# Kernel tuning notes

Measured on AMD Instinct MI355X. Metric: run time of the kernel, lower is better.

The kernel has to match this reference:

```python
import jax, jax.numpy as jnp
import numpy as np

NUM_USERS = 100000
NUM_ITEMS = 50000
NUM_EDGES = 2000000
EMBED_DIM = 64


def setup_inputs() -> dict:
    key = jax.random.key(0)
    k1, k2, k3, k4 = jax.random.split(key, 4)
    return {
        "user_emb": jax.random.normal(k1, (NUM_USERS, EMBED_DIM), dtype=jnp.float32),
        "item_emb": jax.random.normal(k2, (NUM_ITEMS, EMBED_DIM), dtype=jnp.float32),
        "edge_values": jnp.ones((NUM_EDGES,), dtype=jnp.float32),
        "edge_users": jax.random.randint(k3, (NUM_EDGES,), 0, NUM_USERS, dtype=jnp.int32),
        "edge_items": jax.random.randint(k4, (NUM_EDGES,), 0, NUM_ITEMS, dtype=jnp.int32),
        "n_layers": 3,
    }


def reference(user_emb, item_emb, edge_values, edge_users, edge_items, n_layers):
    num_users = user_emb.shape[0]
    num_items = item_emb.shape[0]
    n_total = num_users + num_items

    # Row-normalize by user degree: vals * 1/sqrt(row_sum + 1e-6)  (as in create_adj_matrix)
    row_sum = jax.ops.segment_sum(edge_values, edge_users, num_segments=num_users) + 1e-6
    norm_vals = edge_values * (1.0 / jnp.sqrt(row_sum))[edge_users]

    # Symmetric block adjacency: A[u, U+i] = norm_vals, A[U+i, u] = norm_vals
    items_off = edge_items + num_users
    rows = jnp.concatenate([edge_users, items_off])   # [2E] destination nodes
    cols = jnp.concatenate([items_off, edge_users])   # [2E] source nodes
    vals = jnp.concatenate([norm_vals, norm_vals])    # [2E]

    emb0 = jnp.concatenate([user_emb, item_emb], axis=0)  # [N, D]

    def spmm_layer(e, _):
        # out[r] = sum_{edges e: rows==r} vals * e[cols]
        gathered = vals[:, None] * e[cols]  # [2E, D]
        return jax.ops.segment_sum(gathered, rows, num_segments=n_total), None

    emb, _ = jax.lax.scan(spmm_layer, emb0, None, length=n_layers)
    return emb
```

## Files before the change

### kernel.cpp

```cpp
#include <hip/hip_runtime.h>

#define NUM_USERS 100000
#define NUM_ITEMS 50000
#define NUM_EDGES 2000000
#define EMB_D 64
#define N_TOTAL (NUM_USERS + NUM_ITEMS)
#define TOT_ENTRIES (2 * NUM_EDGES)

#define RPB 512
#define NB ((N_TOTAL + RPB - 1) / RPB)
#define EPB 8192
#define PBLK ((NUM_EDGES + EPB - 1) / EPB)
#define HTOT (NB * PBLK)
#define SCAN_BLKS ((HTOT + 255) / 256)

__device__ __forceinline__ unsigned f32_to_bf16_bits(float f) {
    unsigned u = __float_as_uint(f);
    u += 0x7FFFu + ((u >> 16) & 1u);
    return u >> 16;
}

__global__ __launch_bounds__(256) void part_hist_kernel(
        const int* __restrict__ eu, const int* __restrict__ ei,
        int* __restrict__ histT) {
    __shared__ int h[NB];
    const int t = threadIdx.x;
    for (int i = t; i < NB; i += 256) h[i] = 0;
    __syncthreads();
    const int e0 = blockIdx.x * EPB;
    const int e1 = min(e0 + EPB, NUM_EDGES);
    for (int e = e0 + t; e < e1; e += 256) {
        const int u = eu[e];
        const int iu = NUM_USERS + ei[e];
        atomicAdd(&h[u >> 9], 1);
        atomicAdd(&h[iu >> 9], 1);
    }
    __syncthreads();
    for (int i = t; i < NB; i += 256)
        histT[i * PBLK + blockIdx.x] = h[i];
}

__global__ __launch_bounds__(256) void scanA_kernel(int* __restrict__ histT,
                                                    int* __restrict__ bsum) {
    __shared__ int s[256];
    const int t = threadIdx.x;
    const int i = blockIdx.x * 256 + t;
    int v = (i < HTOT) ? histT[i] : 0;
    s[t] = v;
    __syncthreads();
    for (int off = 1; off < 256; off <<= 1) {
        int x = (t >= off) ? s[t - off] : 0;
        __syncthreads();
        s[t] += x;
        __syncthreads();
    }
    if (i < HTOT) histT[i] = s[t] - v;
    if (t == 255) bsum[blockIdx.x] = s[255];
}

__global__ __launch_bounds__(512) void scanB_kernel(int* __restrict__ bsum) {
    __shared__ int s[512];
    const int t = threadIdx.x;
    int v = (t < SCAN_BLKS) ? bsum[t] : 0;
    s[t] = v;
    __syncthreads();
    for (int off = 1; off < 512; off <<= 1) {
        int x = (t >= off) ? s[t - off] : 0;
        __syncthreads();
        s[t] += x;
        __syncthreads();
    }
    if (t < SCAN_BLKS) bsum[t] = s[t] - v;
}

__global__ __launch_bounds__(256) void scanC_kernel(int* __restrict__ histT,
                                                    const int* __restrict__ bsum) {
    const int i = blockIdx.x * 256 + threadIdx.x;
    if (i < HTOT) histT[i] += bsum[blockIdx.x];
}

__global__ __launch_bounds__(256) void part_scatter_kernel(
        const int* __restrict__ eu, const int* __restrict__ ei,
        const int* __restrict__ histT, unsigned* __restrict__ staging) {
    __shared__ int cur[NB];
    const int t = threadIdx.x;
    for (int i = t; i < NB; i += 256) cur[i] = histT[i * PBLK + blockIdx.x];
    __syncthreads();
    const int e0 = blockIdx.x * EPB;
    const int e1 = min(e0 + EPB, NUM_EDGES);
    for (int e = e0 + t; e < e1; e += 256) {
        const int u = eu[e];
        const int iu = NUM_USERS + ei[e];
        const int p1 = atomicAdd(&cur[u >> 9], 1);
        staging[p1] = ((unsigned)(u & 511) << 18) | (unsigned)iu;
        const int p2 = atomicAdd(&cur[iu >> 9], 1);
        staging[p2] = ((unsigned)(iu & 511) << 18) | (unsigned)u;
    }
}

__global__ __launch_bounds__(512) void bucket_finalize_kernel(
        const unsigned* __restrict__ staging,
        const int* __restrict__ histT,
        unsigned* __restrict__ cw,
        int* __restrict__ row_ptr,
        int* __restrict__ cnt_g,
        float* __restrict__ inv_g) {
    __shared__ int sc[512];
    __shared__ int cur[512];
    __shared__ int span[2];
    const int t = threadIdx.x;
    const int b = blockIdx.x;
    if (t == 0) {
        span[0] = histT[b * PBLK];
        span[1] = (b + 1 < NB) ? histT[(b + 1) * PBLK] : TOT_ENTRIES;
    }
    sc[t] = 0;
    __syncthreads();
    const int base = span[0], end = span[1];
    for (int j = base + t; j < end; j += 512)
        atomicAdd(&sc[staging[j] >> 18], 1);
    __syncthreads();
    const int myc = sc[t];
    for (int off = 1; off < 512; off <<= 1) {
        int x = (t >= off) ? sc[t - off] : 0;
        __syncthreads();
        sc[t] += x;
        __syncthreads();
    }
    const int start = base + sc[t] - myc;
    cur[t] = start;
    const int row = b * RPB + t;
    if (row < N_TOTAL) {
        row_ptr[row] = start;
        cnt_g[row] = myc;
        if (row < NUM_USERS) inv_g[row] = rsqrtf((float)myc + 1e-6f);
    }
    __syncthreads();
    for (int j = base + t; j < end; j += 512) {
        const unsigned v = staging[j];
        const int p = atomicAdd(&cur[v >> 18], 1);
        cw[p] = v & 0x3FFFFu;
    }
}

__global__ __launch_bounds__(256) void convert_kernel(
        const float* __restrict__ user_emb,
        const float* __restrict__ item_emb,
        const float* __restrict__ inv,
        unsigned* __restrict__ x0bf) {
    const int tid = blockIdx.x * blockDim.x + threadIdx.x;
    if (tid >= N_TOTAL * (EMB_D / 2)) return;
    const int row = tid >> 5;
    const int d0 = (tid & 31) << 1;
    float f0, f1, sc;
    if (row < NUM_USERS) {
        const float* p = user_emb + (size_t)row * EMB_D + d0;
        f0 = p[0]; f1 = p[1];
        sc = inv[row];
    } else {
        const float* p = item_emb + (size_t)(row - NUM_USERS) * EMB_D + d0;
        f0 = p[0]; f1 = p[1];
        sc = 1.0f;
    }
    f0 *= sc; f1 *= sc;
    x0bf[tid] = f32_to_bf16_bits(f0) | (f32_to_bf16_bits(f1) << 16);
}

template <int FINAL>
__global__ __launch_bounds__(256) void spmm_kernel(
        const uint4* __restrict__ in_bf,
        const int* __restrict__ row_ptr,
        const int* __restrict__ cnt,
        const unsigned* __restrict__ cw,
        const float* __restrict__ inv,
        uint4* __restrict__ out_bf,
        float* __restrict__ out_f32) {
    const int lane = threadIdx.x & 63;
    const int row = blockIdx.x * 4 + (threadIdx.x >> 6);
    if (row >= N_TOTAL) return;

    const int sub = lane >> 3;
    const int l8 = lane & 7;

    const int start = row_ptr[row];
    const int n = cnt[row];

    float acc[8];
    #pragma unroll
    for (int i = 0; i < 8; i++) acc[i] = 0.0f;

    #pragma unroll 2
    for (int k = 0; k < n; k += 8) {
        const int eidx = k + sub;
        const bool valid = (eidx < n);
        const int col = (int)cw[start + (valid ? eidx : 0)];
        const uint4 q = in_bf[(size_t)col * 8 + l8];
        const float w = valid ? 1.0f : 0.0f;
        acc[0] = fmaf(w, __uint_as_float(q.x << 16),         acc[0]);
        acc[1] = fmaf(w, __uint_as_float(q.x & 0xFFFF0000u), acc[1]);
        acc[2] = fmaf(w, __uint_as_float(q.y << 16),         acc[2]);
        acc[3] = fmaf(w, __uint_as_float(q.y & 0xFFFF0000u), acc[3]);
        acc[4] = fmaf(w, __uint_as_float(q.z << 16),         acc[4]);
        acc[5] = fmaf(w, __uint_as_float(q.z & 0xFFFF0000u), acc[5]);
        acc[6] = fmaf(w, __uint_as_float(q.w << 16),         acc[6]);
        acc[7] = fmaf(w, __uint_as_float(q.w & 0xFFFF0000u), acc[7]);
    }

    #pragma unroll
    for (int m = 32; m >= 8; m >>= 1) {
        #pragma unroll
        for (int i = 0; i < 8; i++) acc[i] += __shfl_xor(acc[i], m);
    }

    if (sub == 0) {
        float sc = 1.0f;
        if (row < NUM_USERS) {
            const float iv = inv[row];
            sc = FINAL ? iv : iv * iv;
        }
        #pragma unroll
        for (int i = 0; i < 8; i++) acc[i] *= sc;
        if (FINAL) {
            float4 a = make_float4(acc[0], acc[1], acc[2], acc[3]);
            float4 b = make_float4(acc[4], acc[5], acc[6], acc[7]);
            float* dst = out_f32 + (size_t)row * EMB_D + 8 * l8;
            *reinterpret_cast<float4*>(dst) = a;
            *reinterpret_cast<float4*>(dst + 4) = b;
        } else {
            uint4 h;
            h.x = f32_to_bf16_bits(acc[0]) | (f32_to_bf16_bits(acc[1]) << 16);
            h.y = f32_to_bf16_bits(acc[2]) | (f32_to_bf16_bits(acc[3]) << 16);
            h.z = f32_to_bf16_bits(acc[4]) | (f32_to_bf16_bits(acc[5]) << 16);
            h.w = f32_to_bf16_bits(acc[6]) | (f32_to_bf16_bits(acc[7]) << 16);
            out_bf[(size_t)row * 8 + l8] = h;
        }
    }
}

extern "C" void kernel_launch(void* const* d_in, const int* in_sizes, int n_in,
                              void* d_out, int out_size, void* d_ws, size_t ws_size,
                              hipStream_t stream) {
    const float* user_emb = (const float*)d_in[0];
    const float* item_emb = (const float*)d_in[1];
    const int*   eu       = (const int*)d_in[3];
    const int*   ei       = (const int*)d_in[4];

    float* out = (float*)d_out;

    char* ws = (char*)d_ws;
    size_t off = 0;
    auto alloc = [&](size_t bytes) {
        char* p = ws + off;
        off = (off + bytes + 511) & ~(size_t)511;
        return p;
    };
    int*      histT   = (int*)     alloc((size_t)HTOT * sizeof(int));
    int*      bsum    = (int*)     alloc((size_t)SCAN_BLKS * sizeof(int));
    int*      row_ptr = (int*)     alloc((size_t)N_TOTAL * sizeof(int));
    int*      cnt     = (int*)     alloc((size_t)N_TOTAL * sizeof(int));
    float*    inv     = (float*)   alloc((size_t)NUM_USERS * sizeof(float));
    unsigned* staging = (unsigned*)alloc((size_t)TOT_ENTRIES * sizeof(unsigned));
    unsigned* cw      = (unsigned*)alloc((size_t)TOT_ENTRIES * sizeof(unsigned));
    unsigned* x0bf    = (unsigned*)alloc((size_t)N_TOTAL * EMB_D * 2);
    unsigned* z1      = (unsigned*)alloc((size_t)N_TOTAL * EMB_D * 2);
    unsigned* z2      = (unsigned*)alloc((size_t)N_TOTAL * EMB_D * 2);

    part_hist_kernel<<<PBLK, 256, 0, stream>>>(eu, ei, histT);
    scanA_kernel<<<SCAN_BLKS, 256, 0, stream>>>(histT, bsum);
    scanB_kernel<<<1, 512, 0, stream>>>(bsum);
    scanC_kernel<<<SCAN_BLKS, 256, 0, stream>>>(histT, bsum);
    part_scatter_kernel<<<PBLK, 256, 0, stream>>>(eu, ei, histT, staging);
    bucket_finalize_kernel<<<NB, 512, 0, stream>>>(staging, histT, cw,
                                                   row_ptr, cnt, inv);

    const int cv_threads = N_TOTAL * (EMB_D / 2);
    convert_kernel<<<(cv_threads + 255) / 256, 256, 0, stream>>>(
        user_emb, item_emb, inv, x0bf);

    const int grid = (N_TOTAL + 3) / 4;

    spmm_kernel<0><<<grid, 256, 0, stream>>>((const uint4*)x0bf, row_ptr, cnt,
                                             cw, inv, (uint4*)z1, nullptr);
    spmm_kernel<0><<<grid, 256, 0, stream>>>((const uint4*)z1, row_ptr, cnt,
                                             cw, inv, (uint4*)z2, nullptr);
    spmm_kernel<1><<<grid, 256, 0, stream>>>((const uint4*)z2, row_ptr, cnt,
                                             cw, inv, nullptr, out);
}
```

Baseline: 310.2 us.

## Process four rows per wavefront in SpMM and vectorize embedding conversion

Each wavefront in the SpMM kernel now handles four destination rows at once. Their gathers are interleaved inside one loop over the maximum row length, which raises memory-level parallelism and gives four times fewer waves and blocks. In exchange, shorter rows do padded work up to the longest of the four, each thread keeps 32 accumulators, and the shuffle reduction grows fourfold. Separately, the convert kernel reads float4 and writes uint2, and intermediate bf16 outputs use nontemporal stores with 32-bit byte-offset addressing.

```diff
diff --git a/kernel.cpp b/kernel.cpp
--- a/kernel.cpp
+++ b/kernel.cpp
@@ -13,6 +13,8 @@
 #define PBLK ((NUM_EDGES + EPB - 1) / EPB)
 #define HTOT (NB * PBLK)
 #define SCAN_BLKS ((HTOT + 255) / 256)
+
+typedef unsigned int nuint4 __attribute__((ext_vector_type(4)));
 
 __device__ __forceinline__ unsigned f32_to_bf16_bits(float f) {
     unsigned u = __float_as_uint(f);
@@ -149,90 +151,120 @@
         const float* __restrict__ inv,
         unsigned* __restrict__ x0bf) {
     const int tid = blockIdx.x * blockDim.x + threadIdx.x;
-    if (tid >= N_TOTAL * (EMB_D / 2)) return;
-    const int row = tid >> 5;
-    const int d0 = (tid & 31) << 1;
-    float f0, f1, sc;
+    if (tid >= N_TOTAL * (EMB_D / 4)) return;
+    const int row = tid >> 4;
+    const int d0 = (tid & 15) << 2;
+    float4 f;
+    float sc;
     if (row < NUM_USERS) {
-        const float* p = user_emb + (size_t)row * EMB_D + d0;
-        f0 = p[0]; f1 = p[1];
+        f = *reinterpret_cast<const float4*>(user_emb + (size_t)row * EMB_D + d0);
         sc = inv[row];
     } else {
-        const float* p = item_emb + (size_t)(row - NUM_USERS) * EMB_D + d0;
-        f0 = p[0]; f1 = p[1];
+        f = *reinterpret_cast<const float4*>(item_emb + (size_t)(row - NUM_USERS) * EMB_D + d0);
         sc = 1.0f;
     }
-    f0 *= sc; f1 *= sc;
-    x0bf[tid] = f32_to_bf16_bits(f0) | (f32_to_bf16_bits(f1) << 16);
+    uint2 o;
+    o.x = f32_to_bf16_bits(f.x * sc) | (f32_to_bf16_bits(f.y * sc) << 16);
+    o.y = f32_to_bf16_bits(f.z * sc) | (f32_to_bf16_bits(f.w * sc) << 16);
+    *reinterpret_cast<uint2*>(x0bf + (size_t)tid * 2) = o;
 }
 
 template <int FINAL>
 __global__ __launch_bounds__(256) void spmm_kernel(
-        const uint4* __restrict__ in_bf,
+        const char* __restrict__ in_base,
         const int* __restrict__ row_ptr,
         const int* __restrict__ cnt,
         const unsigned* __restrict__ cw,
         const float* __restrict__ inv,
-        uint4* __restrict__ out_bf,
+        unsigned* __restrict__ out_bf,
         float* __restrict__ out_f32) {
     const int lane = threadIdx.x & 63;
-    const int row = blockIdx.x * 4 + (threadIdx.x >> 6);
-    if (row >= N_TOTAL) return;
+    const int wv = (blockIdx.x << 2) + (threadIdx.x >> 6);
+    const int row0 = wv << 2;
+    if (row0 >= N_TOTAL) return;
 
     const int sub = lane >> 3;
     const int l8 = lane & 7;
-
-    const int start = row_ptr[row];
-    const int n = cnt[row];
-
-    float acc[8];
+    const unsigned lb = (unsigned)(l8 << 4);
+
+    int st[4], nn[4];
     #pragma unroll
-    for (int i = 0; i < 8; i++) acc[i] = 0.0f;
-
-    #pragma unroll 2
-    for (int k = 0; k < n; k += 8) {
+    for (int c = 0; c < 4; c++) {
+        const int r = row0 + c;
+        if (r < N_TOTAL) { st[c] = row_ptr[r]; nn[c] = cnt[r]; }
+        else             { st[c] = 0;          nn[c] = 0; }
+    }
+    const int nmax = max(max(nn[0], nn[1]), max(nn[2], nn[3]));
+
+    float acc[4][8];
+    #pragma unroll
+    for (int c = 0; c < 4; c++)
+        #pragma unroll
+        for (int i = 0; i < 8; i++) acc[c][i] = 0.0f;
+
+    for (int k = 0; k < nmax; k += 8) {
         const int eidx = k + sub;
-        const bool valid = (eidx < n);
-        const int col = (int)cw[start + (valid ? eidx : 0)];
-        const uint4 q = in_bf[(size_t)col * 8 + l8];
-        const float w = valid ? 1.0f : 0.0f;
-        acc[0] = fmaf(w, __uint_as_float(q.x << 16),         acc[0]);
-        acc[1] = fmaf(w, __uint_as_float(q.x & 0xFFFF0000u), acc[1]);
-        acc[2] = fmaf(w, __uint_as_float(q.y << 16),         acc[2]);
-        acc[3] = fmaf(w, __uint_as_float(q.y & 0xFFFF0000u), acc[3]);
-        acc[4] = fmaf(w, __uint_as_float(q.z << 16),         acc[4]);
-        acc[5] = fmaf(w, __uint_as_float(q.z & 0xFFFF0000u), acc[5]);
-        acc[6] = fmaf(w, __uint_as_float(q.w << 16),         acc[6]);
-        acc[7] = fmaf(w, __uint_as_float(q.w & 0xFFFF0000u), acc[7]);
+        #pragma unroll
+        for (int c = 0; c < 4; c++) {
+            const bool v = (eidx < nn[c]);
+            const unsigned idx = (unsigned)min(st[c] + (v ? eidx : 0), TOT_ENTRIES - 1);
+            const unsigned col = cw[idx];
+            const nuint4 q = *reinterpret_cast<const nuint4*>(in_base + (col * 128u + lb));
+            const float w = v ? 1.0f : 0.0f;
+            acc[c][0] = fmaf(w, __uint_as_float(q.x << 16),         acc[c][0]);
+            acc[c][1] = fmaf(w, __uint_as_float(q.x & 0xFFFF0000u), acc[c][1]);
+            acc[c][2] = fmaf(w, __uint_as_float(q.y << 16),         acc[c][2]);
+            acc[c][3] = fmaf(w, __uint_as_float(q.y & 0xFFFF0000u), acc[c][3]);
+            acc[c][4] = fmaf(w, __uint_as_float(q.z << 16),         acc[c][4]);
+            acc[c][5] = fmaf(w, __uint_as_float(q.z & 0xFFFF0000u), acc[c][5]);
+            acc[c][6] = fmaf(w, __uint_as_float(q.w << 16),         acc[c][6]);
+            acc[c][7] = fmaf(w, __uint_as_float(q.w & 0xFFFF0000u), acc[c][7]);
+        }
     }
 
     #pragma unroll
     for (int m = 32; m >= 8; m >>= 1) {
         #pragma unroll
-        for (int i = 0; i < 8; i++) acc[i] += __shfl_xor(acc[i], m);
-    }
-
-    if (sub == 0) {
-        float sc = 1.0f;
-        if (row < NUM_USERS) {
-            const float iv = inv[row];
-            sc = FINAL ? iv : iv * iv;
-        }
-        #pragma unroll
-        for (int i = 0; i < 8; i++) acc[i] *= sc;
-        if (FINAL) {
-            float4 a = make_float4(acc[0], acc[1], acc[2], acc[3]);
-            float4 b = make_float4(acc[4], acc[5], acc[6], acc[7]);
-            float* dst = out_f32 + (size_t)row * EMB_D + 8 * l8;
-            *reinterpret_cast<float4*>(dst) = a;
-            *reinterpret_cast<float4*>(dst + 4) = b;
-        } else {
-            uint4 h;
-            h.x = f32_to_bf16_bits(acc[0]) | (f32_to_bf16_bits(acc[1]) << 16);
-            h.y = f32_to_bf16_bits(acc[2]) | (f32_to_bf16_bits(acc[3]) << 16);
-            h.z = f32_to_bf16_bits(acc[4]) | (f32_to_bf16_bits(acc[5]) << 16);
-            h.w = f32_to_bf16_bits(acc[6]) | (f32_to_bf16_bits(acc[7]) << 16);
-            out_bf[(size_t)row * 8 + l8] = h;
+        for (int c = 0; c < 4; c++)
+            #pragma unroll
+            for (int i = 0; i < 8; i++)
+                acc[c][i] += __shfl_xor(acc[c][i], m);
+    }
+
+    if (sub < 4) {
+        const int myrow = row0 + sub;
+        if (myrow < N_TOTAL) {
+            float a[8];
+            #pragma unroll
+            for (int i = 0; i < 8; i++) {
+                float x = acc[0][i];
+                x = (sub == 1) ? acc[1][i] : x;
+                x = (sub == 2) ? acc[2][i] : x;
+                x = (sub == 3) ? acc[3][i] : x;
+                a[i] = x;
+            }
+            float sc = 1.0f;
+            if (myrow < NUM_USERS) {
+                const float iv = inv[myrow];
+                sc = FINAL ? iv : iv * iv;
+            }
+            #pragma unroll
+            for (int i = 0; i < 8; i++) a[i] *= sc;
+            if (FINAL) {
+                float4 x = make_float4(a[0], a[1], a[2], a[3]);
+                float4 y = make_float4(a[4], a[5], a[6], a[7]);
+                float* dst = out_f32 + (size_t)myrow * EMB_D + 8 * l8;
+                *reinterpret_cast<float4*>(dst) = x;
+                *reinterpret_cast<float4*>(dst + 4) = y;
+            } else {
+                nuint4 h;
+                h.x = f32_to_bf16_bits(a[0]) | (f32_to_bf16_bits(a[1]) << 16);
+                h.y = f32_to_bf16_bits(a[2]) | (f32_to_bf16_bits(a[3]) << 16);
+                h.z = f32_to_bf16_bits(a[4]) | (f32_to_bf16_bits(a[5]) << 16);
+                h.w = f32_to_bf16_bits(a[6]) | (f32_to_bf16_bits(a[7]) << 16);
+                nuint4* dst = reinterpret_cast<nuint4*>(out_bf + (size_t)myrow * 32 + l8 * 4);
+                __builtin_nontemporal_store(h, dst);
+            }
         }
     }
 }
@@ -273,16 +305,16 @@
     bucket_finalize_kernel<<<NB, 512, 0, stream>>>(staging, histT, cw,
                                                    row_ptr, cnt, inv);
 
-    const int cv_threads = N_TOTAL * (EMB_D / 2);
+    const int cv_threads = N_TOTAL * (EMB_D / 4);
     convert_kernel<<<(cv_threads + 255) / 256, 256, 0, stream>>>(
         user_emb, item_emb, inv, x0bf);
 
-    const int grid = (N_TOTAL + 3) / 4;
-
-    spmm_kernel<0><<<grid, 256, 0, stream>>>((const uint4*)x0bf, row_ptr, cnt,
-                                             cw, inv, (uint4*)z1, nullptr);
-    spmm_kernel<0><<<grid, 256, 0, stream>>>((const uint4*)z1, row_ptr, cnt,
-                                             cw, inv, (uint4*)z2, nullptr);
-    spmm_kernel<1><<<grid, 256, 0, stream>>>((const uint4*)z2, row_ptr, cnt,
+    const int grid = (N_TOTAL + 15) / 16;
+
+    spmm_kernel<0><<<grid, 256, 0, stream>>>((const char*)x0bf, row_ptr, cnt,
+                                             cw, inv, z1, nullptr);
+    spmm_kernel<0><<<grid, 256, 0, stream>>>((const char*)z1, row_ptr, cnt,
+                                             cw, inv, z2, nullptr);
+    spmm_kernel<1><<<grid, 256, 0, stream>>>((const char*)z2, row_ptr, cnt,
                                              cw, inv, nullptr, out);
 }
```

Result: slower. 467.0 us (+50.6%).
